# Kernel optimization log

Measured on AMD Instinct MI355X. Metric: run time of the kernel, lower is better.

## Reference

```python
import jax, jax.numpy as jnp
import numpy as np

NUM_HEADS = 16
EMBED_DIM = 2048
HEAD_DIM = EMBED_DIM // NUM_HEADS
B, S = 2, 2048


def setup_inputs() -> dict:
    key = jax.random.key(0)
    ks = jax.random.split(key, 12)
    E = EMBED_DIM
    scale = 1.0 / np.sqrt(E)  # xavier-ish for square E->E dense
    inp = {
        "x": jax.random.normal(ks[0], (B, S, E), dtype=jnp.float32),
        "sin": jax.random.uniform(ks[1], (1, NUM_HEADS, S, HEAD_DIM), dtype=jnp.float32),
        "cos": jax.random.uniform(ks[2], (1, NUM_HEADS, S, HEAD_DIM), dtype=jnp.float32),
        "mask": jax.random.randint(ks[3], (B, S, S), 0, 2, dtype=jnp.int32),
        "Wq": jax.random.normal(ks[4], (E, E), dtype=jnp.float32) * scale,
        "bq": jnp.zeros((E,), dtype=jnp.float32),
        "Wk": jax.random.normal(ks[5], (E, E), dtype=jnp.float32) * scale,
        "bk": jnp.zeros((E,), dtype=jnp.float32),
        "Wv": jax.random.normal(ks[6], (E, E), dtype=jnp.float32) * scale,
        "bv": jnp.zeros((E,), dtype=jnp.float32),
        "Wo": jax.random.normal(ks[7], (E, E), dtype=jnp.float32) * scale,
        "bo": jnp.zeros((E,), dtype=jnp.float32),
    }
    return inp


def _minus_swap_alternate(t):
    # stack([-t[...,1::2], t[...,::2]], -1).reshape(t.shape)
    return jnp.stack([-t[..., 1::2], t[..., ::2]], axis=-1).reshape(t.shape)


def _forward(x, sin, cos, mask, Wq, bq, Wk, bk, Wv, bv, Wo, bo):
    Bx, Sx, E = x.shape
    H, D = NUM_HEADS, HEAD_DIM
    q = (x @ Wq + bq).reshape(Bx, Sx, H, D).transpose(0, 2, 1, 3)  # (B,H,S,D)
    k = (x @ Wk + bk).reshape(Bx, Sx, H, D).transpose(0, 2, 1, 3)
    v = (x @ Wv + bv).reshape(Bx, Sx, H, D).transpose(0, 2, 1, 3)
    # RoPE applied post-transpose: T = q.shape[1] == H (faithful to source)
    T = q.shape[1]
    s = sin[:, :T, :, :]
    c = cos[:, :T, :, :]
    q = q * c + _minus_swap_alternate(q) * s
    k = k * c + _minus_swap_alternate(k) * s
    m = mask[:, None, :, :]  # expand_mask: (B,S,S) -> (B,1,S,S)
    logits = jnp.einsum("bhqd,bhkd->bhqk", q, k) / jnp.sqrt(jnp.float32(D))
    logits = jnp.where(m == 0, jnp.float32(-9e15), logits)
    attention = jax.nn.softmax(logits, axis=-1)          # first softmax
    values = jnp.matmul(attention, v)                    # (B,H,S,D)
    attention_weights = jax.nn.softmax(attention, axis=-1)  # redundant second softmax
    attn_output = jnp.matmul(attention_weights, values)  # (B,H,S,D)
    attn_output = attn_output.transpose(0, 2, 1, 3).reshape(Bx, Sx, E)
    out = attn_output @ Wo + bo
    return out, attention_weights


def reference(x, sin, cos, mask, Wq, bq, Wk, bk, Wv, bv, Wo, bo):
    return _forward(x, sin, cos, mask, Wq, bq, Wk, bk, Wv, bv, Wo, bo)
```

## Files before the change

kernel.cpp:

```cpp
#include <hip/hip_runtime.h>

typedef unsigned short u16;
typedef unsigned int u32;
typedef __attribute__((ext_vector_type(8))) short short8;
typedef __attribute__((ext_vector_type(4))) float floatx4;

constexpr int Bc = 2, Sc = 2048, Ec = 2048, Hc = 16, Dc = 128;
constexpr int TILE = 128, BK = 32;
constexpr int BUF = TILE * BK;

__device__ __forceinline__ u16 f2bf(float f) {
  u32 u = __builtin_bit_cast(u32, f);
  u = (u + 0x7FFFu + ((u >> 16) & 1u)) >> 16;
  return (u16)u;
}

__device__ __forceinline__ float bf2f(short s) {
  u32 u = ((u32)(u16)s) << 16;
  return __builtin_bit_cast(float, u);
}

__device__ __forceinline__ short8 pack2(float4 a, float4 b) {
  short8 r;
  r[0] = (short)f2bf(a.x); r[1] = (short)f2bf(a.y);
  r[2] = (short)f2bf(a.z); r[3] = (short)f2bf(a.w);
  r[4] = (short)f2bf(b.x); r[5] = (short)f2bf(b.y);
  r[6] = (short)f2bf(b.z); r[7] = (short)f2bf(b.w);
  return r;
}

__device__ __forceinline__ void glds16(const u16* g, u16* l) {
  __builtin_amdgcn_global_load_lds(
      (const __attribute__((address_space(1))) u32*)g,
      (__attribute__((address_space(3))) u32*)l, 16, 0, 0);
}

__device__ __forceinline__ void gemm_core(const u16* __restrict__ A, int lda,
                                          const u16* __restrict__ Bt, int ldb,
                                          int K, int m0, int n0,
                                          u16* smA, u16* smB,
                                          floatx4 (*acc)[4]) {
  const int t = threadIdx.x;
  const int lane = t & 63;
  const int w = t >> 6;
  const int wr = (w >> 1) * 64, wc = (w & 1) * 64;
  const int l15 = lane & 15, q = lane >> 4;

  const int r0 = t >> 2;
  const int c0 = (t & 3) ^ (r0 & 3);
  const u16* A0 = A + (size_t)(m0 + r0) * lda + c0 * 8;
  const u16* A1 = A0 + (size_t)64 * lda;
  const u16* B0 = Bt + (size_t)(n0 + r0) * ldb + c0 * 8;
  const u16* B1 = B0 + (size_t)64 * ldb;
  u16* dA0 = smA + w * 512;
  u16* dA1 = smA + 2048 + w * 512;
  u16* dB0 = smB + w * 512;
  u16* dB1 = smB + 2048 + w * 512;

  for (int k0 = 0; k0 < K; k0 += BK) {
    glds16(A0 + k0, dA0);
    glds16(A1 + k0, dA1);
    glds16(B0 + k0, dB0);
    glds16(B1 + k0, dB1);
    __syncthreads();

    short8 af[4], bfr[4];
    #pragma unroll
    for (int i = 0; i < 4; i++) {
      int ra = wr + i * 16 + l15;
      af[i] = *(const short8*)&smA[ra * BK + ((q ^ (ra & 3)) << 3)];
      int rb = wc + i * 16 + l15;
      bfr[i] = *(const short8*)&smB[rb * BK + ((q ^ (rb & 3)) << 3)];
    }
    #pragma unroll
    for (int mi = 0; mi < 4; mi++)
      #pragma unroll
      for (int ni = 0; ni < 4; ni++)
        acc[mi][ni] = __builtin_amdgcn_mfma_f32_16x16x32_bf16(af[mi], bfr[ni], acc[mi][ni], 0, 0, 0);
    __syncthreads();
  }
}

__global__ __launch_bounds__(256) void transpose_w(
    const float* __restrict__ Wq, const float* __restrict__ Wk,
    const float* __restrict__ Wv, const float* __restrict__ Wo,
    u16* __restrict__ WT, u16* __restrict__ WoT) {
  __shared__ float tile[32][33];
  const int z = blockIdx.z;
  const float* W = (z == 0) ? Wq : (z == 1) ? Wk : (z == 2) ? Wv : Wo;
  u16* dst = (z < 3) ? (WT + (size_t)z * Ec * Ec) : WoT;
  const int n0 = blockIdx.x * 32, k0 = blockIdx.y * 32;
  const int tx = threadIdx.x, ty = threadIdx.y;
  #pragma unroll
  for (int i = 0; i < 4; i++)
    tile[ty + 8 * i][tx] = W[(size_t)(k0 + ty + 8 * i) * Ec + n0 + tx];
  __syncthreads();
  #pragma unroll
  for (int i = 0; i < 4; i++)
    dst[(size_t)(n0 + ty + 8 * i) * Ec + k0 + tx] = f2bf(tile[tx][ty + 8 * i]);
}

__global__ __launch_bounds__(256) void xcvt_kernel(const float* __restrict__ x,
                                                   u16* __restrict__ xb,
                                                   float* __restrict__ s1) {
  const int i = blockIdx.x * 256 + threadIdx.x;
  const float4 f0 = ((const float4*)x)[(size_t)i * 2];
  const float4 f1 = ((const float4*)x)[(size_t)i * 2 + 1];
  *(short8*)&xb[(size_t)i * 8] = pack2(f0, f1);
  if (blockIdx.x < 64)
    ((float4*)s1)[i] = make_float4(0.f, 0.f, 0.f, 0.f);
}

__global__ __launch_bounds__(256) void qkv_kernel(
    const u16* __restrict__ xb, const u16* __restrict__ WT,
    const float* __restrict__ bq, const float* __restrict__ bk, const float* __restrict__ bv,
    const float* __restrict__ sinp, const float* __restrict__ cosp,
    u16* __restrict__ qr, u16* __restrict__ kr, u16* __restrict__ vT) {
  __shared__ __align__(16) u16 smA[BUF];
  __shared__ __align__(16) u16 smB[BUF];
  floatx4 acc[4][4] = {};
  const int m0 = blockIdx.y * TILE, n0 = blockIdx.x * TILE;
  gemm_core(xb, Ec, WT, Ec, Ec, m0, n0, smA, smB, acc);

  const int t = threadIdx.x, lane = t & 63, w = t >> 6;
  const int wr = (w >> 1) * 64, wc = (w & 1) * 64, l15 = lane & 15, q = lane >> 4;
  #pragma unroll
  for (int mi = 0; mi < 4; mi++) {
    #pragma unroll
    for (int ni = 0; ni < 4; ni++) {
      const int gcol = n0 + wc + ni * 16 + l15;
      const int which = gcol >> 11;
      const int e = gcol & 2047, h = e >> 7, d = e & 127;
      const float* bp = (which == 0) ? bq : (which == 1) ? bk : bv;
      const float bias = bp[e];
      #pragma unroll
      for (int rr = 0; rr < 4; rr++) {
        const int grow = m0 + wr + mi * 16 + q * 4 + rr;
        const int b = grow >> 11, s = grow & 2047;
        float val = acc[mi][ni][rr] + bias;
        float pv = __shfl_xor(val, 1);
        if (which < 2) {
          const size_t sc = ((size_t)h * Sc + s) * Dc + d;
          const float c = cosp[sc], sn = sinp[sc];
          const float o = val * c + ((d & 1) ? pv : -pv) * sn;
          u16* dst = which ? kr : qr;
          dst[(((size_t)b * Hc + h) * Sc + s) * Dc + d] = f2bf(o);
        } else {
          vT[(((size_t)b * Hc + h) * Dc + d) * Sc + s] = f2bf(val);
        }
      }
    }
  }
}

__global__ __launch_bounds__(256) void logits_kernel(
    const u16* __restrict__ qr, const u16* __restrict__ kr,
    const int* __restrict__ maskp, u16* __restrict__ Pbuf, float* __restrict__ s1) {
  __shared__ __align__(16) u16 smA[BUF];
  __shared__ __align__(16) u16 smB[BUF];
  floatx4 acc[4][4] = {};
  const int z = blockIdx.z;
  const int m0 = blockIdx.y * TILE, n0 = blockIdx.x * TILE;
  gemm_core(qr + (size_t)z * Sc * Dc, Dc, kr + (size_t)z * Sc * Dc, Dc, Dc, m0, n0, smA, smB, acc);

  u16* Pp = Pbuf + (size_t)z * Sc * Sc;
  const int b = z >> 4;
  const float scale = 0.08838834764831845f;
  const int t = threadIdx.x, lane = t & 63, w = t >> 6;
  const int wr = (w >> 1) * 64, wc = (w & 1) * 64, l15 = lane & 15, q = lane >> 4;
  float rs[4][4];
  #pragma unroll
  for (int mi = 0; mi < 4; mi++)
    #pragma unroll
    for (int rr = 0; rr < 4; rr++) rs[mi][rr] = 0.f;

  #pragma unroll
  for (int mi = 0; mi < 4; mi++)
    #pragma unroll
    for (int ni = 0; ni < 4; ni++) {
      const int gcol = n0 + wc + ni * 16 + l15;
      #pragma unroll
      for (int rr = 0; rr < 4; rr++) {
        const int grow = m0 + wr + mi * 16 + q * 4 + rr;
        const int mv = maskp[((size_t)b * Sc + grow) * Sc + gcol];
        const float val = mv ? acc[mi][ni][rr] * scale : -9.0e15f;
        const float pe = __expf(val);
        rs[mi][rr] += pe;
        Pp[(size_t)grow * Sc + gcol] = f2bf(pe);
      }
    }
  #pragma unroll
  for (int mi = 0; mi < 4; mi++)
    #pragma unroll
    for (int rr = 0; rr < 4; rr++) {
      float xs = rs[mi][rr];
      xs += __shfl_xor(xs, 1);
      xs += __shfl_xor(xs, 2);
      xs += __shfl_xor(xs, 4);
      xs += __shfl_xor(xs, 8);
      if (l15 == 0)
        atomicAdd(&s1[z * Sc + m0 + wr + mi * 16 + q * 4 + rr], xs);
    }
}

__global__ __launch_bounds__(256) void av_kernel(
    const u16* __restrict__ P, const u16* __restrict__ vT,
    const float* __restrict__ s1, u16* __restrict__ valT, float* __restrict__ s2) {
  __shared__ __align__(16) u16 smA[64 * BK];
  __shared__ __align__(16) u16 smB[TILE * BK];
  floatx4 acc[4][2] = {};
  const int z = blockIdx.z;
  const int m0 = blockIdx.y * 64;
  const int t = threadIdx.x, lane = t & 63, w = t >> 6;
  const int wc = w * 32;
  const int l15 = lane & 15, q = lane >> 4;

  const int r0 = t >> 2;
  const int c0 = (t & 3) ^ (r0 & 3);
  const u16* Pb = P + (size_t)z * Sc * Sc;
  const u16* A0 = Pb + (size_t)(m0 + r0) * Sc + c0 * 8;
  const u16* Bb = vT + (size_t)z * Dc * Sc;
  const u16* B0 = Bb + (size_t)r0 * Sc + c0 * 8;
  const u16* B1 = B0 + (size_t)64 * Sc;
  u16* dA0 = smA + w * 512;
  u16* dB0 = smB + w * 512;
  u16* dB1 = smB + 2048 + w * 512;

  const float inv1a = 1.0f / s1[z * Sc + m0 + r0];
  float s2a = 0.0f;

  for (int k0 = 0; k0 < Sc; k0 += BK) {
    glds16(A0 + k0, dA0);
    glds16(B0 + k0, dB0);
    glds16(B1 + k0, dB1);
    __syncthreads();

    short8 af[4], bfr[2];
    #pragma unroll
    for (int i = 0; i < 4; i++) {
      int ra = i * 16 + l15;
      af[i] = *(const short8*)&smA[ra * BK + ((q ^ (ra & 3)) << 3)];
    }
    #pragma unroll
    for (int i = 0; i < 2; i++) {
      int rb = wc + i * 16 + l15;
      bfr[i] = *(const short8*)&smB[rb * BK + ((q ^ (rb & 3)) << 3)];
    }
    short8 pa = *(const short8*)&smA[t * 8];

    #pragma unroll
    for (int mi = 0; mi < 4; mi++)
      #pragma unroll
      for (int ni = 0; ni < 2; ni++)
        acc[mi][ni] = __builtin_amdgcn_mfma_f32_16x16x32_bf16(af[mi], bfr[ni], acc[mi][ni], 0, 0, 0);

    #pragma unroll
    for (int j = 0; j < 8; j++)
      s2a += __expf(bf2f(pa[j]) * inv1a);
    __syncthreads();
  }

  s2a += __shfl_xor(s2a, 1);
  s2a += __shfl_xor(s2a, 2);
  if ((t & 3) == 0) s2[z * Sc + m0 + r0] = s2a;

  float iv[4][4];
  #pragma unroll
  for (int mi = 0; mi < 4; mi++)
    #pragma unroll
    for (int rr = 0; rr < 4; rr++)
      iv[mi][rr] = 1.0f / s1[z * Sc + m0 + mi * 16 + q * 4 + rr];

  u16* C = valT + (size_t)z * Dc * Sc;
  #pragma unroll
  for (int mi = 0; mi < 4; mi++)
    #pragma unroll
    for (int ni = 0; ni < 2; ni++) {
      const int gcol = wc + ni * 16 + l15;
      #pragma unroll
      for (int rr = 0; rr < 4; rr++) {
        const int grow = m0 + mi * 16 + q * 4 + rr;
        C[(size_t)gcol * Sc + grow] = f2bf(acc[mi][ni][rr] * iv[mi][rr]);
      }
    }
}

__global__ __launch_bounds__(256) void wv_kernel(
    const u16* __restrict__ P, const u16* __restrict__ valT,
    const float* __restrict__ s1, const float* __restrict__ s2,
    float* __restrict__ a2out, u16* __restrict__ aox) {
  __shared__ __align__(16) u16 smA[64 * BK];
  __shared__ __align__(16) u16 smB[TILE * BK];
  floatx4 acc[4][2] = {};
  const int z = blockIdx.z;
  const int m0 = blockIdx.y * 64;
  const int t = threadIdx.x, lane = t & 63, w = t >> 6;
  const int wc = w * 32;
  const int l15 = lane & 15, q = lane >> 4;

  const int r = t >> 2;
  const int cg = t & 3;
  const u16* Bb = valT + (size_t)z * Dc * Sc;
  const u16* B0 = Bb + (size_t)r * Sc + ((cg ^ (r & 3)) * 8);
  const u16* B1 = B0 + (size_t)64 * Sc;
  u16* dB0 = smB + w * 512;
  u16* dB1 = smB + 2048 + w * 512;

  const u16* Prow = P + (size_t)z * Sc * Sc + (size_t)(m0 + r) * Sc + cg * 8;
  float* Orow = a2out + (size_t)z * Sc * Sc + (size_t)(m0 + r) * Sc + cg * 8;
  const float inv1 = 1.0f / s1[z * Sc + m0 + r];
  const float inv2 = 1.0f / s2[z * Sc + m0 + r];

  for (int k0 = 0; k0 < Sc; k0 += BK) {
    glds16(B0 + k0, dB0);
    glds16(B1 + k0, dB1);

    short8 p0 = *(const short8*)(Prow + k0);
    float4 f[2];
    float* e = (float*)f;
    #pragma unroll
    for (int j = 0; j < 8; j++) e[j] = __expf(bf2f(p0[j]) * inv1) * inv2;
    ((float4*)(Orow + k0))[0] = f[0];
    ((float4*)(Orow + k0))[1] = f[1];
    short8 a0 = pack2(f[0], f[1]);
    *(short8*)&smA[r * BK + ((cg ^ (r & 3)) << 3)] = a0;
    __syncthreads();

    short8 af[4], bfr[2];
    #pragma unroll
    for (int i = 0; i < 4; i++) {
      int ra = i * 16 + l15;
      af[i] = *(const short8*)&smA[ra * BK + ((q ^ (ra & 3)) << 3)];
    }
    #pragma unroll
    for (int i = 0; i < 2; i++) {
      int rb = wc + i * 16 + l15;
      bfr[i] = *(const short8*)&smB[rb * BK + ((q ^ (rb & 3)) << 3)];
    }
    #pragma unroll
    for (int mi = 0; mi < 4; mi++)
      #pragma unroll
      for (int ni = 0; ni < 2; ni++)
        acc[mi][ni] = __builtin_amdgcn_mfma_f32_16x16x32_bf16(af[mi], bfr[ni], acc[mi][ni], 0, 0, 0);
    __syncthreads();
  }

  const int b = z >> 4, h = z & 15;
  #pragma unroll
  for (int mi = 0; mi < 4; mi++)
    #pragma unroll
    for (int ni = 0; ni < 2; ni++) {
      const int gcol = wc + ni * 16 + l15;
      #pragma unroll
      for (int rr = 0; rr < 4; rr++) {
        const int grow = m0 + mi * 16 + q * 4 + rr;
        aox[((size_t)b * Sc + grow) * Ec + h * Dc + gcol] = f2bf(acc[mi][ni][rr]);
      }
    }
}

__global__ __launch_bounds__(256) void out_kernel(
    const u16* __restrict__ aox, const u16* __restrict__ WoT,
    const float* __restrict__ bo, float* __restrict__ outp) {
  __shared__ __align__(16) u16 smA[BUF];
  __shared__ __align__(16) u16 smB[BUF];
  floatx4 acc[4][4] = {};
  const int m0 = blockIdx.y * TILE, n0 = blockIdx.x * TILE;
  gemm_core(aox, Ec, WoT, Ec, Ec, m0, n0, smA, smB, acc);

  const int t = threadIdx.x, lane = t & 63, w = t >> 6;
  const int wr = (w >> 1) * 64, wc = (w & 1) * 64, l15 = lane & 15, q = lane >> 4;
  #pragma unroll
  for (int mi = 0; mi < 4; mi++)
    #pragma unroll
    for (int ni = 0; ni < 4; ni++) {
      const int gcol = n0 + wc + ni * 16 + l15;
      const float bias = bo[gcol];
      #pragma unroll
      for (int rr = 0; rr < 4; rr++) {
        const int grow = m0 + wr + mi * 16 + q * 4 + rr;
        outp[(size_t)grow * Ec + gcol] = acc[mi][ni][rr] + bias;
      }
    }
}

extern "C" void kernel_launch(void* const* d_in, const int* in_sizes, int n_in,
                              void* d_out, int out_size, void* d_ws, size_t ws_size,
                              hipStream_t stream) {
  const float* x     = (const float*)d_in[0];
  const float* sinp  = (const float*)d_in[1];
  const float* cosp  = (const float*)d_in[2];
  const int*   maskp = (const int*)d_in[3];
  const float* Wq    = (const float*)d_in[4];
  const float* bq    = (const float*)d_in[5];
  const float* Wk    = (const float*)d_in[6];
  const float* bk    = (const float*)d_in[7];
  const float* Wv    = (const float*)d_in[8];
  const float* bv    = (const float*)d_in[9];
  const float* Wo    = (const float*)d_in[10];
  const float* bo    = (const float*)d_in[11];

  float* out0  = (float*)d_out;
  float* attnL = out0 + (size_t)Bc * Sc * Ec;

  u16* wsp  = (u16*)d_ws;
  u16* WT   = wsp;
  u16* WoT  = WT + (size_t)3 * Ec * Ec;
  u16* xb   = WoT + (size_t)Ec * Ec;
  u16* qr   = xb + (size_t)Bc * Sc * Ec;
  u16* kr   = qr + (size_t)Bc * Hc * Sc * Dc;
  u16* vT   = kr + (size_t)Bc * Hc * Sc * Dc;
  u16* valT = vT + (size_t)Bc * Hc * Sc * Dc;
  u16* aox  = valT + (size_t)Bc * Hc * Sc * Dc;
  float* s1 = (float*)(aox + (size_t)Bc * Sc * Ec);
  float* s2 = s1 + (size_t)Bc * Hc * Sc;
  u16* Pbuf = (u16*)(s2 + (size_t)Bc * Hc * Sc);

  transpose_w<<<dim3(64, 64, 4), dim3(32, 8), 0, stream>>>(Wq, Wk, Wv, Wo, WT, WoT);
  xcvt_kernel<<<dim3(4096), 256, 0, stream>>>(x, xb, s1);
  qkv_kernel<<<dim3(48, 32), 256, 0, stream>>>(xb, WT, bq, bk, bv, sinp, cosp, qr, kr, vT);
  logits_kernel<<<dim3(16, 16, 32), 256, 0, stream>>>(qr, kr, maskp, Pbuf, s1);
  av_kernel<<<dim3(1, 32, 32), 256, 0, stream>>>(Pbuf, vT, s1, valT, s2);
  wv_kernel<<<dim3(1, 32, 32), 256, 0, stream>>>(Pbuf, valT, s1, s2, attnL, aox);
  out_kernel<<<dim3(16, 32), 256, 0, stream>>>(aox, WoT, bo, out0);
}
```

Before: 1.307 ms.

## Double GEMM K-tile depth to 64 with 8-way LDS swizzle and XCD-aware block remap

Raises the shared-memory K step from 32 to 64 in every GEMM-like kernel, so each barrier pair covers two MFMA k-substeps and half as many global-to-LDS load rounds and __syncthreads are needed. The XOR swizzle widens to 8 chunks, and the load mapping, softmax-sum and exp/pack loops in av/wv are rewritten to handle two rows or two chunks per thread. The qkv and out GEMMs also remap block indices so consecutive blocks scattered round-robin across XCDs work on nearby tiles, aiming for better L2 reuse. LDS use per block doubles, which may reduce occupancy.

```diff
diff --git a/kernel.cpp b/kernel.cpp
--- a/kernel.cpp
+++ b/kernel.cpp
@@ -6,8 +6,7 @@
 typedef __attribute__((ext_vector_type(4))) float floatx4;
 
 constexpr int Bc = 2, Sc = 2048, Ec = 2048, Hc = 16, Dc = 128;
-constexpr int TILE = 128, BK = 32;
-constexpr int BUF = TILE * BK;
+constexpr int TILE = 128, BK = 64;
 
 __device__ __forceinline__ u16 f2bf(float f) {
   u32 u = __builtin_bit_cast(u32, f);
@@ -46,37 +45,37 @@
   const int wr = (w >> 1) * 64, wc = (w & 1) * 64;
   const int l15 = lane & 15, q = lane >> 4;
 
-  const int r0 = t >> 2;
-  const int c0 = (t & 3) ^ (r0 & 3);
-  const u16* A0 = A + (size_t)(m0 + r0) * lda + c0 * 8;
-  const u16* A1 = A0 + (size_t)64 * lda;
-  const u16* B0 = Bt + (size_t)(n0 + r0) * ldb + c0 * 8;
-  const u16* B1 = B0 + (size_t)64 * ldb;
-  u16* dA0 = smA + w * 512;
-  u16* dA1 = smA + 2048 + w * 512;
-  u16* dB0 = smB + w * 512;
-  u16* dB1 = smB + 2048 + w * 512;
+  const int r0 = t >> 3;
+  const int c0 = (t & 7) ^ (r0 & 7);
+  const u16* Ap = A + (size_t)(m0 + r0) * lda + c0 * 8;
+  const u16* Bp = Bt + (size_t)(n0 + r0) * ldb + c0 * 8;
+  u16* dA = smA + w * 512;
+  u16* dB = smB + w * 512;
 
   for (int k0 = 0; k0 < K; k0 += BK) {
-    glds16(A0 + k0, dA0);
-    glds16(A1 + k0, dA1);
-    glds16(B0 + k0, dB0);
-    glds16(B1 + k0, dB1);
-    __syncthreads();
-
-    short8 af[4], bfr[4];
-    #pragma unroll
-    for (int i = 0; i < 4; i++) {
-      int ra = wr + i * 16 + l15;
-      af[i] = *(const short8*)&smA[ra * BK + ((q ^ (ra & 3)) << 3)];
-      int rb = wc + i * 16 + l15;
-      bfr[i] = *(const short8*)&smB[rb * BK + ((q ^ (rb & 3)) << 3)];
-    }
-    #pragma unroll
-    for (int mi = 0; mi < 4; mi++)
-      #pragma unroll
-      for (int ni = 0; ni < 4; ni++)
-        acc[mi][ni] = __builtin_amdgcn_mfma_f32_16x16x32_bf16(af[mi], bfr[ni], acc[mi][ni], 0, 0, 0);
+    #pragma unroll
+    for (int j = 0; j < 4; j++) {
+      glds16(Ap + (size_t)(32 * j) * lda + k0, dA + j * 2048);
+      glds16(Bp + (size_t)(32 * j) * ldb + k0, dB + j * 2048);
+    }
+    __syncthreads();
+
+    #pragma unroll
+    for (int ks = 0; ks < 2; ks++) {
+      short8 af[4], bfr[4];
+      #pragma unroll
+      for (int i = 0; i < 4; i++) {
+        int ra = wr + i * 16 + l15;
+        af[i] = *(const short8*)&smA[ra * BK + (((ks * 4 + q) ^ (ra & 7)) << 3)];
+        int rb = wc + i * 16 + l15;
+        bfr[i] = *(const short8*)&smB[rb * BK + (((ks * 4 + q) ^ (rb & 7)) << 3)];
+      }
+      #pragma unroll
+      for (int mi = 0; mi < 4; mi++)
+        #pragma unroll
+        for (int ni = 0; ni < 4; ni++)
+          acc[mi][ni] = __builtin_amdgcn_mfma_f32_16x16x32_bf16(af[mi], bfr[ni], acc[mi][ni], 0, 0, 0);
+    }
     __syncthreads();
   }
 }
@@ -116,10 +115,12 @@
     const float* __restrict__ bq, const float* __restrict__ bk, const float* __restrict__ bv,
     const float* __restrict__ sinp, const float* __restrict__ cosp,
     u16* __restrict__ qr, u16* __restrict__ kr, u16* __restrict__ vT) {
-  __shared__ __align__(16) u16 smA[BUF];
-  __shared__ __align__(16) u16 smB[BUF];
+  __shared__ __align__(16) u16 smA[TILE * BK];
+  __shared__ __align__(16) u16 smB[TILE * BK];
   floatx4 acc[4][4] = {};
-  const int m0 = blockIdx.y * TILE, n0 = blockIdx.x * TILE;
+  const int lin = blockIdx.y * 48 + blockIdx.x;
+  const int swz = (lin & 7) * 192 + (lin >> 3);
+  const int m0 = (swz / 48) * TILE, n0 = (swz % 48) * TILE;
   gemm_core(xb, Ec, WT, Ec, Ec, m0, n0, smA, smB, acc);
 
   const int t = threadIdx.x, lane = t & 63, w = t >> 6;
@@ -156,8 +157,8 @@
 __global__ __launch_bounds__(256) void logits_kernel(
     const u16* __restrict__ qr, const u16* __restrict__ kr,
     const int* __restrict__ maskp, u16* __restrict__ Pbuf, float* __restrict__ s1) {
-  __shared__ __align__(16) u16 smA[BUF];
-  __shared__ __align__(16) u16 smB[BUF];
+  __shared__ __align__(16) u16 smA[TILE * BK];
+  __shared__ __align__(16) u16 smB[TILE * BK];
   floatx4 acc[4][4] = {};
   const int z = blockIdx.z;
   const int m0 = blockIdx.y * TILE, n0 = blockIdx.x * TILE;
@@ -207,7 +208,7 @@
     const u16* __restrict__ P, const u16* __restrict__ vT,
     const float* __restrict__ s1, u16* __restrict__ valT, float* __restrict__ s2) {
   __shared__ __align__(16) u16 smA[64 * BK];
-  __shared__ __align__(16) u16 smB[TILE * BK];
+  __shared__ __align__(16) u16 smB[128 * BK];
   floatx4 acc[4][2] = {};
   const int z = blockIdx.z;
   const int m0 = blockIdx.y * 64;
@@ -215,54 +216,63 @@
   const int wc = w * 32;
   const int l15 = lane & 15, q = lane >> 4;
 
-  const int r0 = t >> 2;
-  const int c0 = (t & 3) ^ (r0 & 3);
+  const int r0 = t >> 3;
+  const int c0 = (t & 7) ^ (r0 & 7);
   const u16* Pb = P + (size_t)z * Sc * Sc;
-  const u16* A0 = Pb + (size_t)(m0 + r0) * Sc + c0 * 8;
-  const u16* Bb = vT + (size_t)z * Dc * Sc;
-  const u16* B0 = Bb + (size_t)r0 * Sc + c0 * 8;
-  const u16* B1 = B0 + (size_t)64 * Sc;
-  u16* dA0 = smA + w * 512;
-  u16* dB0 = smB + w * 512;
-  u16* dB1 = smB + 2048 + w * 512;
+  const u16* Ap = Pb + (size_t)(m0 + r0) * Sc + c0 * 8;
+  const u16* Bp = vT + (size_t)z * Dc * Sc + (size_t)r0 * Sc + c0 * 8;
+  u16* dA = smA + w * 512;
+  u16* dB = smB + w * 512;
 
   const float inv1a = 1.0f / s1[z * Sc + m0 + r0];
-  float s2a = 0.0f;
+  const float inv1b = 1.0f / s1[z * Sc + m0 + r0 + 32];
+  float s2a = 0.0f, s2b = 0.0f;
 
   for (int k0 = 0; k0 < Sc; k0 += BK) {
-    glds16(A0 + k0, dA0);
-    glds16(B0 + k0, dB0);
-    glds16(B1 + k0, dB1);
-    __syncthreads();
-
-    short8 af[4], bfr[2];
-    #pragma unroll
-    for (int i = 0; i < 4; i++) {
-      int ra = i * 16 + l15;
-      af[i] = *(const short8*)&smA[ra * BK + ((q ^ (ra & 3)) << 3)];
-    }
-    #pragma unroll
-    for (int i = 0; i < 2; i++) {
-      int rb = wc + i * 16 + l15;
-      bfr[i] = *(const short8*)&smB[rb * BK + ((q ^ (rb & 3)) << 3)];
-    }
+    glds16(Ap + k0, dA);
+    glds16(Ap + (size_t)32 * Sc + k0, dA + 2048);
+    #pragma unroll
+    for (int j = 0; j < 4; j++)
+      glds16(Bp + (size_t)(32 * j) * Sc + k0, dB + j * 2048);
+    __syncthreads();
+
     short8 pa = *(const short8*)&smA[t * 8];
-
-    #pragma unroll
-    for (int mi = 0; mi < 4; mi++)
-      #pragma unroll
-      for (int ni = 0; ni < 2; ni++)
-        acc[mi][ni] = __builtin_amdgcn_mfma_f32_16x16x32_bf16(af[mi], bfr[ni], acc[mi][ni], 0, 0, 0);
-
-    #pragma unroll
-    for (int j = 0; j < 8; j++)
+    short8 pb = *(const short8*)&smA[t * 8 + 2048];
+
+    #pragma unroll
+    for (int ks = 0; ks < 2; ks++) {
+      short8 af[4], bfr[2];
+      #pragma unroll
+      for (int i = 0; i < 4; i++) {
+        int ra = i * 16 + l15;
+        af[i] = *(const short8*)&smA[ra * BK + (((ks * 4 + q) ^ (ra & 7)) << 3)];
+      }
+      #pragma unroll
+      for (int i = 0; i < 2; i++) {
+        int rb = wc + i * 16 + l15;
+        bfr[i] = *(const short8*)&smB[rb * BK + (((ks * 4 + q) ^ (rb & 7)) << 3)];
+      }
+      #pragma unroll
+      for (int mi = 0; mi < 4; mi++)
+        #pragma unroll
+        for (int ni = 0; ni < 2; ni++)
+          acc[mi][ni] = __builtin_amdgcn_mfma_f32_16x16x32_bf16(af[mi], bfr[ni], acc[mi][ni], 0, 0, 0);
+    }
+
+    #pragma unroll
+    for (int j = 0; j < 8; j++) {
       s2a += __expf(bf2f(pa[j]) * inv1a);
+      s2b += __expf(bf2f(pb[j]) * inv1b);
+    }
     __syncthreads();
   }
 
-  s2a += __shfl_xor(s2a, 1);
-  s2a += __shfl_xor(s2a, 2);
-  if ((t & 3) == 0) s2[z * Sc + m0 + r0] = s2a;
+  s2a += __shfl_xor(s2a, 1); s2a += __shfl_xor(s2a, 2); s2a += __shfl_xor(s2a, 4);
+  s2b += __shfl_xor(s2b, 1); s2b += __shfl_xor(s2b, 2); s2b += __shfl_xor(s2b, 4);
+  if ((t & 7) == 0) {
+    s2[z * Sc + m0 + r0] = s2a;
+    s2[z * Sc + m0 + r0 + 32] = s2b;
+  }
 
   float iv[4][4];
   #pragma unroll
@@ -290,7 +300,7 @@
     const float* __restrict__ s1, const float* __restrict__ s2,
     float* __restrict__ a2out, u16* __restrict__ aox) {
   __shared__ __align__(16) u16 smA[64 * BK];
-  __shared__ __align__(16) u16 smB[TILE * BK];
+  __shared__ __align__(16) u16 smB[128 * BK];
   floatx4 acc[4][2] = {};
   const int z = blockIdx.z;
   const int m0 = blockIdx.y * 64;
@@ -299,49 +309,57 @@
   const int l15 = lane & 15, q = lane >> 4;
 
   const int r = t >> 2;
-  const int cg = t & 3;
-  const u16* Bb = valT + (size_t)z * Dc * Sc;
-  const u16* B0 = Bb + (size_t)r * Sc + ((cg ^ (r & 3)) * 8);
-  const u16* B1 = B0 + (size_t)64 * Sc;
-  u16* dB0 = smB + w * 512;
-  u16* dB1 = smB + 2048 + w * 512;
-
-  const u16* Prow = P + (size_t)z * Sc * Sc + (size_t)(m0 + r) * Sc + cg * 8;
-  float* Orow = a2out + (size_t)z * Sc * Sc + (size_t)(m0 + r) * Sc + cg * 8;
+  const int cg2 = (t & 3) * 2;
+  const int r0b = t >> 3;
+  const int c0b = (t & 7) ^ (r0b & 7);
+  const u16* Bp = valT + (size_t)z * Dc * Sc + (size_t)r0b * Sc + c0b * 8;
+  u16* dB = smB + w * 512;
+
+  const u16* Prow = P + (size_t)z * Sc * Sc + (size_t)(m0 + r) * Sc + cg2 * 8;
+  float* Orow = a2out + (size_t)z * Sc * Sc + (size_t)(m0 + r) * Sc + cg2 * 8;
   const float inv1 = 1.0f / s1[z * Sc + m0 + r];
   const float inv2 = 1.0f / s2[z * Sc + m0 + r];
 
   for (int k0 = 0; k0 < Sc; k0 += BK) {
-    glds16(B0 + k0, dB0);
-    glds16(B1 + k0, dB1);
+    #pragma unroll
+    for (int j = 0; j < 4; j++)
+      glds16(Bp + (size_t)(32 * j) * Sc + k0, dB + j * 2048);
 
     short8 p0 = *(const short8*)(Prow + k0);
-    float4 f[2];
+    short8 p1 = *(const short8*)(Prow + k0 + 8);
+    float4 f[4];
     float* e = (float*)f;
     #pragma unroll
     for (int j = 0; j < 8; j++) e[j] = __expf(bf2f(p0[j]) * inv1) * inv2;
-    ((float4*)(Orow + k0))[0] = f[0];
-    ((float4*)(Orow + k0))[1] = f[1];
+    #pragma unroll
+    for (int j = 0; j < 8; j++) e[8 + j] = __expf(bf2f(p1[j]) * inv1) * inv2;
+    #pragma unroll
+    for (int j = 0; j < 4; j++) ((float4*)(Orow + k0))[j] = f[j];
     short8 a0 = pack2(f[0], f[1]);
-    *(short8*)&smA[r * BK + ((cg ^ (r & 3)) << 3)] = a0;
-    __syncthreads();
-
-    short8 af[4], bfr[2];
-    #pragma unroll
-    for (int i = 0; i < 4; i++) {
-      int ra = i * 16 + l15;
-      af[i] = *(const short8*)&smA[ra * BK + ((q ^ (ra & 3)) << 3)];
-    }
-    #pragma unroll
-    for (int i = 0; i < 2; i++) {
-      int rb = wc + i * 16 + l15;
-      bfr[i] = *(const short8*)&smB[rb * BK + ((q ^ (rb & 3)) << 3)];
-    }
-    #pragma unroll
-    for (int mi = 0; mi < 4; mi++)
-      #pragma unroll
-      for (int ni = 0; ni < 2; ni++)
-        acc[mi][ni] = __builtin_amdgcn_mfma_f32_16x16x32_bf16(af[mi], bfr[ni], acc[mi][ni], 0, 0, 0);
+    short8 a1v = pack2(f[2], f[3]);
+    *(short8*)&smA[r * BK + (((cg2 + 0) ^ (r & 7)) << 3)] = a0;
+    *(short8*)&smA[r * BK + (((cg2 + 1) ^ (r & 7)) << 3)] = a1v;
+    __syncthreads();
+
+    #pragma unroll
+    for (int ks = 0; ks < 2; ks++) {
+      short8 af[4], bfr[2];
+      #pragma unroll
+      for (int i = 0; i < 4; i++) {
+        int ra = i * 16 + l15;
+        af[i] = *(const short8*)&smA[ra * BK + (((ks * 4 + q) ^ (ra & 7)) << 3)];
+      }
+      #pragma unroll
+      for (int i = 0; i < 2; i++) {
+        int rb = wc + i * 16 + l15;
+        bfr[i] = *(const short8*)&smB[rb * BK + (((ks * 4 + q) ^ (rb & 7)) << 3)];
+      }
+      #pragma unroll
+      for (int mi = 0; mi < 4; mi++)
+        #pragma unroll
+        for (int ni = 0; ni < 2; ni++)
+          acc[mi][ni] = __builtin_amdgcn_mfma_f32_16x16x32_bf16(af[mi], bfr[ni], acc[mi][ni], 0, 0, 0);
+    }
     __syncthreads();
   }
 
@@ -362,10 +380,12 @@
 __global__ __launch_bounds__(256) void out_kernel(
     const u16* __restrict__ aox, const u16* __restrict__ WoT,
     const float* __restrict__ bo, float* __restrict__ outp) {
-  __shared__ __align__(16) u16 smA[BUF];
-  __shared__ __align__(16) u16 smB[BUF];
+  __shared__ __align__(16) u16 smA[TILE * BK];
+  __shared__ __align__(16) u16 smB[TILE * BK];
   floatx4 acc[4][4] = {};
-  const int m0 = blockIdx.y * TILE, n0 = blockIdx.x * TILE;
+  const int lin = blockIdx.y * 16 + blockIdx.x;
+  const int swz = (lin & 7) * 64 + (lin >> 3);
+  const int m0 = (swz / 16) * TILE, n0 = (swz % 16) * TILE;
   gemm_core(aox, Ec, WoT, Ec, Ec, m0, n0, smA, smB, acc);
 
   const int t = threadIdx.x, lane = t & 63, w = t >> 6;
```

Result: no change. 1.298 ms (-0.6%).
